# Kernel tuning notes

Hardware: AMD Instinct MI355X
Metric: run time of the kernel (lower is better)

## Reference

```python
import jax, jax.numpy as jnp
import numpy as np

B, N, L, C, H = 8, 300, 4096, 256, 8
DH = C // H  # 32; doubled to 64 after concat with pos/sine embeddings


def _linear_params(key, fan_in, fan_out):
    kw, kb = jax.random.split(key)
    bound = 1.0 / np.sqrt(fan_in)
    W = jax.random.uniform(kw, (fan_out, fan_in), jnp.float32, -bound, bound)
    b = jax.random.uniform(kb, (fan_out,), jnp.float32, -bound, bound)
    return W, b


def setup_inputs() -> dict:
    key = jax.random.key(0)
    ks = jax.random.split(key, 13)
    inp = {
        "query": jax.random.normal(ks[0], (B, N, C), jnp.float32),
        "key": jax.random.normal(ks[1], (B, L, C), jnp.float32),
        "value": jax.random.normal(ks[2], (B, L, C), jnp.float32),
        "query_pos": jax.random.normal(ks[3], (B, N, C), jnp.float32),
        "key_pos": jax.random.normal(ks[4], (B, L, C), jnp.float32),
        "query_sine_embed": jax.random.normal(ks[5], (B, N, C), jnp.float32),
    }
    names = ["qc", "qp", "qs", "kc", "kp", "v", "o"]
    for i, nm in enumerate(names):
        W, b = _linear_params(ks[6 + i], C, C)
        inp[f"W{nm}"] = W
        inp[f"b{nm}"] = b
    return inp


def reference(query, key, value, query_pos, key_pos, query_sine_embed,
              Wqc, bqc, Wqp, bqp, Wqs, bqs, Wkc, bkc, Wkp, bkp, Wv, bv, Wo, bo):
    lin = lambda x, W, b: jnp.einsum("bnc,dc->bnd", x, W) + b
    qc = lin(query, Wqc, bqc)                  # (B, N, C)
    kc = lin(key, Wkc, bkc)                    # (B, L, C)
    v = lin(value, Wv, bv)                     # (B, L, C)
    kp = lin(key_pos, Wkp, bkp)                # (B, L, C)
    qp = lin(query_pos, Wqp, bqp)              # is_first=True branch
    q = qc + qp
    k = kc + kp
    qs = lin(query_sine_embed, Wqs, bqs)
    # split heads and concat content with positional/sine embedding -> head dim 2*DH
    q = jnp.concatenate([q.reshape(B, N, H, DH), qs.reshape(B, N, H, DH)], axis=3)   # (B,N,H,2DH)
    k = jnp.concatenate([k.reshape(B, L, H, DH), kp.reshape(B, L, H, DH)], axis=3)   # (B,L,H,2DH)
    vh = v.reshape(B, L, H, DH)
    scale = (2 * DH) ** -0.5
    attn = jnp.einsum("bnhd,blhd->bhnl", q * scale, k)      # (B,H,N,L)
    attn = jax.nn.softmax(attn, axis=-1)
    out = jnp.einsum("bhnl,blhd->bnhd", attn, vh).reshape(B, N, C)
    out = jnp.einsum("bnc,dc->bnd", out, Wo) + bo
    return query + out  # identity = query
```

## Files before the change

### kernel.cpp

```cpp
#include <hip/hip_runtime.h>
#include <hip/hip_bf16.h>

using bf8_t = __attribute__((ext_vector_type(8))) short;
using bf4_t = __attribute__((ext_vector_type(4))) short;
using u16x4 = __attribute__((ext_vector_type(4))) unsigned short;
using f32x4 = __attribute__((ext_vector_type(4))) float;

constexpr int B_   = 8;
constexpr int N_   = 300;
constexpr int L_   = 4096;
constexpr int C_   = 256;
constexpr int H_   = 8;
constexpr int NPAD = 320;
constexpr int QT_  = 5;
constexpr int SPL_ = 4;
constexpr int TPS_ = 16;
constexpr float SCALE = 0.18033688011112042f;

__device__ __forceinline__ unsigned short f2b(float f) {
  unsigned u = __float_as_uint(f);
  u += 0x7FFFu + ((u >> 16) & 1u);
  return (unsigned short)(u >> 16);
}

__device__ __forceinline__ void stage_cvt16(unsigned short* dst, const float* src) {
#pragma unroll
  for (int half = 0; half < 2; ++half) {
    f32x4 x0 = *(const f32x4*)(src + half * 8);
    f32x4 x1 = *(const f32x4*)(src + half * 8 + 4);
    bf8_t v;
#pragma unroll
    for (int j = 0; j < 4; ++j) { v[j] = (short)f2b(x0[j]); v[4 + j] = (short)f2b(x1[j]); }
    *(bf8_t*)(dst + half * 8) = v;
  }
}

__device__ __forceinline__ void gload_lds16(const void* g, void* l) {
  __builtin_amdgcn_global_load_lds(
      (const __attribute__((address_space(1))) unsigned int*)g,
      (__attribute__((address_space(3))) unsigned int*)l, 16, 0, 0);
}

__device__ __forceinline__ unsigned cvt_pk_bf16(float lo, float hi) {
  unsigned r;
  asm("v_cvt_pk_bf16_f32 %0, %1, %2" : "=v"(r) : "v"(lo), "v"(hi));
  return r;
}

__global__ __launch_bounds__(256) void wcvt_k(
    const float* __restrict__ W0, const float* __restrict__ W1, const float* __restrict__ W2,
    const float* __restrict__ W3, const float* __restrict__ W4, const float* __restrict__ W5,
    unsigned short* __restrict__ Wsw)
{
  const float* W[6] = {W0, W1, W2, W3, W4, W5};
  const int kt = blockIdx.x, i = blockIdx.y;
  const int d = threadIdx.x;
  const float* src = W[i] + (size_t)d * C_ + kt * 64;
  unsigned short* dst = Wsw + ((size_t)(i * 4 + kt) * 256 + d) * 64;
#pragma unroll
  for (int g = 0; g < 8; ++g) {
    f32x4 a = *(const f32x4*)(src + g * 8);
    f32x4 b = *(const f32x4*)(src + g * 8 + 4);
    bf8_t v;
#pragma unroll
    for (int j = 0; j < 4; ++j) { v[j] = (short)f2b(a[j]); v[4 + j] = (short)f2b(b[j]); }
    *(bf8_t*)(dst + (g ^ (d & 7)) * 8) = v;
  }
}

__global__ __launch_bounds__(256, 2) void kvproj_k(
    const float* __restrict__ xp, const float* __restrict__ xk, const float* __restrict__ xv,
    const unsigned short* __restrict__ Wsw,
    const float* __restrict__ bkp, const float* __restrict__ bkc, const float* __restrict__ bv,
    unsigned short* __restrict__ Kc, unsigned short* __restrict__ Kp, unsigned short* __restrict__ Vt)
{
  __shared__ __align__(16) unsigned short Al[2][64 * 64];
  __shared__ __align__(16) unsigned short Bl[2][256 * 64];
  const int tid = threadIdx.x, lane = tid & 63, wv = tid >> 6;
  const int fr = lane & 15, fg = lane >> 4;
  const int row0 = blockIdx.x * 64;
  const int b = row0 >> 12, ll0 = row0 & (L_ - 1);
  const float* Ax[3] = {xp, xk, xv};

  const int sr = tid >> 2, sc = (tid & 3) * 16;
  const int ag = sc >> 3;

  f32x4 acc[16];

  auto stageB = [&](int step, int buf) {
    const char* bsrc = (const char*)Wsw + (size_t)step * 32768;
    char* bdst = (char*)&Bl[buf][0];
#pragma unroll
    for (int c = 0; c < 8; ++c) {
      const int off = c * 4096 + wv * 1024 + lane * 16;
      gload_lds16(bsrc + off, bdst + off);
    }
  };
  auto stageA_load = [&](int step, f32x4* ar) {
    const int i = step >> 2, kt = step & 3;
    const float* src = Ax[i] + ((size_t)(row0 + sr)) * C_ + kt * 64 + sc;
#pragma unroll
    for (int j = 0; j < 4; ++j) ar[j] = *(const f32x4*)(src + j * 4);
  };
  auto stageA_write = [&](int buf, const f32x4* ar) {
    unsigned short* base = &Al[buf][sr * 64];
    bf8_t v0, v1;
#pragma unroll
    for (int j = 0; j < 4; ++j) {
      v0[j] = (short)f2b(ar[0][j]); v0[4 + j] = (short)f2b(ar[1][j]);
      v1[j] = (short)f2b(ar[2][j]); v1[4 + j] = (short)f2b(ar[3][j]);
    }
    *(bf8_t*)(base + ((ag ^ (sr & 7)) * 8))       = v0;
    *(bf8_t*)(base + (((ag | 1) ^ (sr & 7)) * 8)) = v1;
  };

  {
    f32x4 a0[4];
    stageA_load(0, a0);
    stageB(0, 0);
    stageA_write(0, a0);
  }
  __syncthreads();

  int cur = 0;
  const int xrow = wv * 16 + fr;
  const int l_out = ll0 + wv * 16 + fr;
  for (int step = 0; step < 12; ++step) {
    const int i = step >> 2, kt = step & 3;
    if (kt == 0 && i != 1) {
#pragma unroll
      for (int nt = 0; nt < 16; ++nt) acc[nt] = (f32x4){0.f, 0.f, 0.f, 0.f};
    }
    const int nxt = cur ^ 1;
    f32x4 arn[4];
    if (step < 11) {
      stageA_load(step + 1, arn);
      stageB(step + 1, nxt);
    }
    const unsigned short* Ab = &Al[cur][0];
    const unsigned short* Bb = &Bl[cur][0];
#pragma unroll
    for (int kh = 0; kh < 2; ++kh) {
      const int gx = (4 * kh + fg) ^ (fr & 7);
      bf8_t xf = *(const bf8_t*)(Ab + xrow * 64 + gx * 8);
#pragma unroll
      for (int nt = 0; nt < 16; ++nt) {
        bf8_t wf = *(const bf8_t*)(Bb + (nt * 16 + fr) * 64 + gx * 8);
        acc[nt] = __builtin_amdgcn_mfma_f32_16x16x32_bf16(wf, xf, acc[nt], 0, 0, 0);
      }
    }
    if (kt == 3) {
      if (i < 2) {
        unsigned short* outp = (i == 0) ? Kp : Kc;
#pragma unroll
        for (int nt = 0; nt < 16; ++nt) {
          const int d0 = nt * 16 + fg * 4;
          f32x4 bb = *(const f32x4*)(bkp + d0);
          if (i == 1) bb += *(const f32x4*)(bkc + d0);
          u16x4 v;
#pragma unroll
          for (int r = 0; r < 4; ++r) v[r] = f2b(acc[nt][r] + bb[r]);
          *(u16x4*)(outp + ((size_t)(b * H_ + (d0 >> 5)) * L_ + l_out) * 32 + (d0 & 31)) = v;
        }
      } else {
        __syncthreads();
        unsigned short* T = (unsigned short*)&Bl[0][0];
#pragma unroll
        for (int nt = 0; nt < 16; ++nt) {
          const int d0 = nt * 16 + fg * 4;
          f32x4 bb = *(const f32x4*)(bv + d0);
#pragma unroll
          for (int r = 0; r < 4; ++r)
            T[(d0 + r) * 68 + wv * 16 + fr] = f2b(acc[nt][r] + bb[r]);
        }
        __syncthreads();
        const int d = tid, h2 = d >> 5, dh2 = d & 31;
        unsigned short* dst = Vt + ((size_t)(b * H_ + h2) * 32 + dh2) * L_ + ll0;
#pragma unroll
        for (int j = 0; j < 16; ++j)
          *(u16x4*)(dst + j * 4) = *(const u16x4*)(T + d * 68 + j * 4);
      }
    }
    if (step < 11) stageA_write(nxt, arn);
    __syncthreads();
    cur = nxt;
  }
}

__global__ __launch_bounds__(256, 2) void qproj_k(
    const float* __restrict__ xp, const float* __restrict__ xq, const float* __restrict__ xs,
    const unsigned short* __restrict__ Wsw,
    const float* __restrict__ bqp, const float* __restrict__ bqc, const float* __restrict__ bqs,
    unsigned short* __restrict__ Qcat)
{
  __shared__ __align__(16) unsigned short Al[2][64 * 64];
  __shared__ __align__(16) unsigned short Bl[2][256 * 64];
  const int tid = threadIdx.x, lane = tid & 63, wv = tid >> 6;
  const int fr = lane & 15, fg = lane >> 4;
  const int b = blockIdx.x / 5, n0 = (blockIdx.x % 5) * 64;
  const float* Ax[3] = {xp, xq, xs};

  const int sr = tid >> 2, sc = (tid & 3) * 16;
  const int ag = sc >> 3;
  const bool arow_ok = (n0 + sr) < N_;

  f32x4 acc[16];

  auto stageB = [&](int step, int buf) {
    const char* bsrc = (const char*)Wsw + (size_t)(12 + step) * 32768;
    char* bdst = (char*)&Bl[buf][0];
#pragma unroll
    for (int c = 0; c < 8; ++c) {
      const int off = c * 4096 + wv * 1024 + lane * 16;
      gload_lds16(bsrc + off, bdst + off);
    }
  };
  auto stageA_load = [&](int step, f32x4* ar) {
    const int i = step >> 2, kt = step & 3;
    if (arow_ok) {
      const float* src = Ax[i] + ((size_t)b * N_ + n0 + sr) * C_ + kt * 64 + sc;
#pragma unroll
      for (int j = 0; j < 4; ++j) ar[j] = *(const f32x4*)(src + j * 4);
    } else {
#pragma unroll
      for (int j = 0; j < 4; ++j) ar[j] = (f32x4){0.f, 0.f, 0.f, 0.f};
    }
  };
  auto stageA_write = [&](int buf, const f32x4* ar) {
    unsigned short* base = &Al[buf][sr * 64];
    bf8_t v0, v1;
#pragma unroll
    for (int j = 0; j < 4; ++j) {
      v0[j] = (short)f2b(ar[0][j]); v0[4 + j] = (short)f2b(ar[1][j]);
      v1[j] = (short)f2b(ar[2][j]); v1[4 + j] = (short)f2b(ar[3][j]);
    }
    *(bf8_t*)(base + ((ag ^ (sr & 7)) * 8))       = v0;
    *(bf8_t*)(base + (((ag | 1) ^ (sr & 7)) * 8)) = v1;
  };

  {
    f32x4 a0[4];
    stageA_load(0, a0);
    stageB(0, 0);
    stageA_write(0, a0);
  }
  __syncthreads();

  int cur = 0;
  const int xrow = wv * 16 + fr;
  const int n_out = n0 + wv * 16 + fr;
  const bool ok = n_out < N_;
  for (int step = 0; step < 12; ++step) {
    if (step == 0 || step == 8) {
#pragma unroll
      for (int nt = 0; nt < 16; ++nt) acc[nt] = (f32x4){0.f, 0.f, 0.f, 0.f};
    }
    const int nxt = cur ^ 1;
    f32x4 arn[4];
    if (step < 11) {
      stageA_load(step + 1, arn);
      stageB(step + 1, nxt);
    }
    const unsigned short* Ab = &Al[cur][0];
    const unsigned short* Bb = &Bl[cur][0];
#pragma unroll
    for (int kh = 0; kh < 2; ++kh) {
      const int gx = (4 * kh + fg) ^ (fr & 7);
      bf8_t xf = *(const bf8_t*)(Ab + xrow * 64 + gx * 8);
#pragma unroll
      for (int nt = 0; nt < 16; ++nt) {
        bf8_t wf = *(const bf8_t*)(Bb + (nt * 16 + fr) * 64 + gx * 8);
        acc[nt] = __builtin_amdgcn_mfma_f32_16x16x32_bf16(wf, xf, acc[nt], 0, 0, 0);
      }
    }
    if (step == 7 || step == 11) {
      const int off = (step == 7) ? 0 : 32;
#pragma unroll
      for (int nt = 0; nt < 16; ++nt) {
        const int d0 = nt * 16 + fg * 4;
        f32x4 bb;
        if (step == 7) bb = *(const f32x4*)(bqp + d0) + *(const f32x4*)(bqc + d0);
        else           bb = *(const f32x4*)(bqs + d0);
        u16x4 v;
#pragma unroll
        for (int r = 0; r < 4; ++r) v[r] = ok ? f2b((acc[nt][r] + bb[r]) * SCALE) : (unsigned short)0;
        *(u16x4*)(Qcat + ((size_t)(b * H_ + (d0 >> 5)) * NPAD + n_out) * 64 + off + (d0 & 31)) = v;
      }
    }
    if (step < 11) stageA_write(nxt, arn);
    __syncthreads();
    cur = nxt;
  }
}

__global__ __launch_bounds__(256, 5) void attn_k(
    const unsigned short* __restrict__ Qcat, const unsigned short* __restrict__ Kc,
    const unsigned short* __restrict__ Kp, const unsigned short* __restrict__ Vt,
    float* __restrict__ PO, float* __restrict__ PM, float* __restrict__ PLs)
{
  __shared__ __align__(16) unsigned short Kcl[2][64 * 32];
  __shared__ __align__(16) unsigned short Kpl[2][64 * 32];
  __shared__ __align__(16) unsigned short Vp[2][32][72];
  const int x = blockIdx.x;
  const int qt = x >> 8;
  const int rem = x & 255;
  const int s = rem & (SPL_ - 1);
  const int h = (rem >> 2) & (H_ - 1);
  const int b = rem >> 5;
  const int n0 = qt * 64;
  const int tid = threadIdx.x, lane = tid & 63, wv = tid >> 6;
  const int fr = lane & 15, fg = lane >> 4;

  const unsigned short* Qb = Qcat + ((size_t)b * H_ + h) * NPAD * 64;
  bf8_t qf[2];
  {
    const int qrow = n0 + wv * 16 + fr;
    qf[0] = *(const bf8_t*)&Qb[(size_t)qrow * 64 + 8 * fg];
    qf[1] = *(const bf8_t*)&Qb[(size_t)qrow * 64 + 32 + 8 * fg];
  }
  float m_r = -1e30f, l_r = 0.f;
  f32x4 o[2] = {};

  const unsigned short* KcB = Kc + ((size_t)b * H_ + h) * L_ * 32;
  const unsigned short* KpB = Kp + ((size_t)b * H_ + h) * L_ * 32;
  const unsigned short* VB  = Vt + ((size_t)b * H_ + h) * 32 * (size_t)L_;

  const int koff = tid * 16;
  const int vd = tid >> 3, vc = (tid & 7) * 8;

  auto stageK = [&](int t, int buf) {
    gload_lds16((const char*)KcB + (size_t)t * 4096 + koff, (char*)&Kcl[buf][0] + koff);
    gload_lds16((const char*)KpB + (size_t)t * 4096 + koff, (char*)&Kpl[buf][0] + koff);
  };

  const int t0 = s * TPS_, t1 = t0 + TPS_;

  stageK(t0, 0);
  bf8_t vreg = *(const bf8_t*)(VB + (size_t)vd * L_ + t0 * 64 + vc);

  int cur = 0;
  for (int t = t0; t < t1; ++t) {
    *(bf8_t*)&Vp[cur][vd][vc] = vreg;
    __syncthreads();
    if (t + 1 < t1) {
      stageK(t + 1, cur ^ 1);
      vreg = *(const bf8_t*)(VB + (size_t)vd * L_ + (t + 1) * 64 + vc);
    }
    f32x4 sc[4] = {};
#pragma unroll
    for (int nf = 0; nf < 4; ++nf) {
      const int kro = (nf * 16 + fr) * 32 + 8 * fg;
      bf8_t kf0 = *(const bf8_t*)&Kcl[cur][kro];
      bf8_t kf1 = *(const bf8_t*)&Kpl[cur][kro];
      sc[nf] = __builtin_amdgcn_mfma_f32_16x16x32_bf16(kf0, qf[0], sc[nf], 0, 0, 0);
      sc[nf] = __builtin_amdgcn_mfma_f32_16x16x32_bf16(kf1, qf[1], sc[nf], 0, 0, 0);
    }
    float mx = fmaxf(fmaxf(sc[0][0], sc[0][1]), fmaxf(sc[0][2], sc[0][3]));
#pragma unroll
    for (int nf = 1; nf < 4; ++nf)
      mx = fmaxf(mx, fmaxf(fmaxf(sc[nf][0], sc[nf][1]), fmaxf(sc[nf][2], sc[nf][3])));
    mx = fmaxf(mx, __shfl_xor(mx, 16));
    mx = fmaxf(mx, __shfl_xor(mx, 32));
    const float mnew = fmaxf(m_r, mx);
    const float corr = exp2f(m_r - mnew);
    float ps = 0.f;
#pragma unroll
    for (int nf = 0; nf < 4; ++nf)
#pragma unroll
      for (int r = 0; r < 4; ++r) {
        const float p = exp2f(sc[nf][r] - mnew);
        sc[nf][r] = p;
        ps += p;
      }
    ps += __shfl_xor(ps, 16);
    ps += __shfl_xor(ps, 32);
    l_r = l_r * corr + ps;
    m_r = mnew;
#pragma unroll
    for (int r = 0; r < 4; ++r) { o[0][r] *= corr; o[1][r] *= corr; }
    unsigned pw[8];
#pragma unroll
    for (int nf = 0; nf < 4; ++nf) {
      pw[2 * nf]     = cvt_pk_bf16(sc[nf][0], sc[nf][1]);
      pw[2 * nf + 1] = cvt_pk_bf16(sc[nf][2], sc[nf][3]);
    }
#pragma unroll
    for (int kh = 0; kh < 2; ++kh) {
      union { unsigned u[4]; bf8_t v; } pu;
      pu.u[0] = pw[4 * kh];     pu.u[1] = pw[4 * kh + 1];
      pu.u[2] = pw[4 * kh + 2]; pu.u[3] = pw[4 * kh + 3];
      const bf8_t pf = pu.v;
#pragma unroll
      for (int df = 0; df < 2; ++df) {
        const unsigned short* vrow = &Vp[cur][df * 16 + fr][0];
        bf4_t va = *(const bf4_t*)(vrow + kh * 32 + fg * 4);
        bf4_t vb = *(const bf4_t*)(vrow + kh * 32 + 16 + fg * 4);
        bf8_t vf;
#pragma unroll
        for (int j = 0; j < 4; ++j) { vf[j] = va[j]; vf[4 + j] = vb[j]; }
        o[df] = __builtin_amdgcn_mfma_f32_16x16x32_bf16(vf, pf, o[df], 0, 0, 0);
      }
    }
    cur ^= 1;
  }
  const int rec = (((b * H_) + h) * QT_ + qt) * SPL_ + s;
  const int q = wv * 16 + fr;
  if (fg == 0) {
    PM [rec * 64 + q] = m_r;
    PLs[rec * 64 + q] = l_r;
  }
#pragma unroll
  for (int df = 0; df < 2; ++df)
    *(f32x4*)(PO + ((size_t)rec * 64 + q) * 32 + df * 16 + fg * 4) = o[df];
}

__global__ __launch_bounds__(256) void combine_k(
    const float* __restrict__ PO, const float* __restrict__ PM, const float* __restrict__ PLs,
    unsigned short* __restrict__ aout)
{
  const int qt = blockIdx.x, h = blockIdx.y, b = blockIdx.z;
  const int tid = threadIdx.x;
  const int row = tid >> 2, dh0 = (tid & 3) * 8;
  const int rec0 = (((b * H_) + h) * QT_ + qt) * SPL_;
  float m[SPL_], w[SPL_];
  float M = -1e30f;
#pragma unroll
  for (int s = 0; s < SPL_; ++s) { m[s] = PM[(rec0 + s) * 64 + row]; M = fmaxf(M, m[s]); }
  float denom = 0.f;
#pragma unroll
  for (int s = 0; s < SPL_; ++s) {
    w[s] = exp2f(m[s] - M);
    denom += w[s] * PLs[(rec0 + s) * 64 + row];
  }
  float num[8] = {};
#pragma unroll
  for (int s = 0; s < SPL_; ++s) {
    const float* po = PO + ((size_t)(rec0 + s) * 64 + row) * 32 + dh0;
    f32x4 a = *(const f32x4*)po;
    f32x4 c = *(const f32x4*)(po + 4);
#pragma unroll
    for (int j = 0; j < 4; ++j) { num[j] += w[s] * a[j]; num[4 + j] += w[s] * c[j]; }
  }
  const int n = qt * 64 + row;
  if (n < N_) {
    const float inv = 1.f / denom;
    bf8_t v;
#pragma unroll
    for (int j = 0; j < 8; ++j) v[j] = (short)f2b(num[j] * inv);
    *(bf8_t*)(aout + ((size_t)b * NPAD + n) * C_ + h * 32 + dh0) = v;
  }
}

__global__ __launch_bounds__(256) void oproj_k(
    const unsigned short* __restrict__ aout, const float* __restrict__ Wo,
    const float* __restrict__ bo, const float* __restrict__ query,
    float* __restrict__ out)
{
  __shared__ __align__(16) unsigned short Al[64][72];
  __shared__ __align__(16) unsigned short Bl[64][72];
  const int b = blockIdx.z, n0 = blockIdx.y * 64, d0 = blockIdx.x * 64;
  const int tid = threadIdx.x, lane = tid & 63, wv = tid >> 6;
  const int wm = wv >> 1, wn = wv & 1;
  const int sr = tid >> 2, sc = (tid & 3) * 16;
  const int fr = lane & 15, fg = lane >> 4;
  f32x4 acc[2][2] = {};

  for (int kt = 0; kt < 4; ++kt) {
    const int k0 = kt * 64;
    {
      const unsigned short* src = aout + ((size_t)b * NPAD + n0 + sr) * C_ + k0 + sc;
      *(bf8_t*)&Al[sr][sc]     = *(const bf8_t*)src;
      *(bf8_t*)&Al[sr][sc + 8] = *(const bf8_t*)(src + 8);
    }
    stage_cvt16(&Bl[sr][sc], Wo + (size_t)(d0 + sr) * C_ + k0 + sc);
    __syncthreads();
#pragma unroll
    for (int kh = 0; kh < 2; ++kh) {
      const int ko = kh * 32 + 8 * fg;
      bf8_t af[2], bq[2];
#pragma unroll
      for (int m = 0; m < 2; ++m) {
        af[m] = *(const bf8_t*)&Al[wm * 32 + m * 16 + fr][ko];
        bq[m] = *(const bf8_t*)&Bl[wn * 32 + m * 16 + fr][ko];
      }
#pragma unroll
      for (int m = 0; m < 2; ++m)
#pragma unroll
        for (int n = 0; n < 2; ++n)
          acc[m][n] = __builtin_amdgcn_mfma_f32_16x16x32_bf16(af[m], bq[n], acc[m][n], 0, 0, 0);
    }
    __syncthreads();
  }
#pragma unroll
  for (int m = 0; m < 2; ++m)
#pragma unroll
    for (int nn = 0; nn < 2; ++nn) {
      const int d = d0 + wn * 32 + nn * 16 + fr;
      const float bb = bo[d];
#pragma unroll
      for (int r = 0; r < 4; ++r) {
        const int n = n0 + wm * 32 + m * 16 + fg * 4 + r;
        if (n < N_) {
          const size_t gi = ((size_t)b * N_ + n) * C_ + d;
          out[gi] = acc[m][nn][r] + bb + query[gi];
        }
      }
    }
}

extern "C" void kernel_launch(void* const* d_in, const int* in_sizes, int n_in,
                              void* d_out, int out_size, void* d_ws, size_t ws_size,
                              hipStream_t stream)
{
  const float* query = (const float*)d_in[0];
  const float* key   = (const float*)d_in[1];
  const float* value = (const float*)d_in[2];
  const float* qpos  = (const float*)d_in[3];
  const float* kpos  = (const float*)d_in[4];
  const float* qsine = (const float*)d_in[5];
  const float* Wqc = (const float*)d_in[6];  const float* bqc = (const float*)d_in[7];
  const float* Wqp = (const float*)d_in[8];  const float* bqp = (const float*)d_in[9];
  const float* Wqs = (const float*)d_in[10]; const float* bqs = (const float*)d_in[11];
  const float* Wkc = (const float*)d_in[12]; const float* bkc = (const float*)d_in[13];
  const float* Wkp = (const float*)d_in[14]; const float* bkp = (const float*)d_in[15];
  const float* Wv  = (const float*)d_in[16]; const float* bv  = (const float*)d_in[17];
  const float* Wo  = (const float*)d_in[18]; const float* bo  = (const float*)d_in[19];

  const size_t qcat_b = (size_t)B_ * H_ * NPAD * 64 * 2;
  const size_t kc_b   = (size_t)B_ * H_ * L_ * 32 * 2;
  const size_t kp_b   = kc_b;
  const size_t vt_b   = kc_b;
  const size_t aout_b = (size_t)B_ * NPAD * C_ * 2;
  const size_t nrec   = (size_t)B_ * H_ * QT_ * SPL_;
  const size_t po_b   = nrec * 64 * 32 * 4;
  const size_t pm_b   = nrec * 64 * 4;
  const size_t pl_b   = nrec * 64 * 4;
  const size_t wsw_b  = (size_t)24 * 256 * 64 * 2;
  if (ws_size < qcat_b + kc_b + kp_b + vt_b + aout_b + po_b + pm_b + pl_b + wsw_b) return;
  char* ws = (char*)d_ws;
  unsigned short* Qcat = (unsigned short*)(ws);
  unsigned short* Kc   = (unsigned short*)(ws + qcat_b);
  unsigned short* Kp   = (unsigned short*)(ws + qcat_b + kc_b);
  unsigned short* Vt   = (unsigned short*)(ws + qcat_b + kc_b + kp_b);
  unsigned short* aout = (unsigned short*)(ws + qcat_b + kc_b + kp_b + vt_b);
  float* PO  = (float*)(ws + qcat_b + kc_b + kp_b + vt_b + aout_b);
  float* PM  = (float*)(ws + qcat_b + kc_b + kp_b + vt_b + aout_b + po_b);
  float* PLs = (float*)(ws + qcat_b + kc_b + kp_b + vt_b + aout_b + po_b + pm_b);
  unsigned short* Wsw = (unsigned short*)(ws + qcat_b + kc_b + kp_b + vt_b + aout_b + po_b + pm_b + pl_b);
  float* out = (float*)d_out;

  wcvt_k   <<<dim3(4, 6),                256, 0, stream>>>(Wkp, Wkc, Wv, Wqp, Wqc, Wqs, Wsw);
  qproj_k  <<<dim3(B_ * QT_),            256, 0, stream>>>(qpos, query, qsine, Wsw, bqp, bqc, bqs, Qcat);
  kvproj_k <<<dim3(512),                 256, 0, stream>>>(kpos, key, value, Wsw, bkp, bkc, bv, Kc, Kp, Vt);
  attn_k   <<<dim3(QT_ * SPL_ * B_ * H_), 256, 0, stream>>>(Qcat, Kc, Kp, Vt, PO, PM, PLs);
  combine_k<<<dim3(QT_, 8, 8),           256, 0, stream>>>(PO, PM, PLs, aout);
  oproj_k  <<<dim3(4, QT_, 8),           256, 0, stream>>>(aout, Wo, bo, query, out);
}
```

Measured before the change: 138.7 us.

## Split K/V projections across grid via score algebra and retile kvproj

The kernel uses the identity q·(kc+kp) + qs·kp = q·kc + (q+qs)·kp. Kc now stores only the kc projection, and the second half of Qcat carries q+qs instead of qs alone. This removes the accumulation dependency between the kp and kc projections, so kvproj_k launches a 512x3 grid with one projection per block. Each block uses 32-wide K steps, 4x4 MFMA tiles per wave, a smaller shared buffer and higher occupancy. The trade-off is more blocks that each re-stage the activation tile, plus a second weight-conversion kernel with a new 32-column swizzled layout.

```diff
diff --git a/kernel.cpp b/kernel.cpp
--- a/kernel.cpp
+++ b/kernel.cpp
@@ -49,14 +49,13 @@
 
 __global__ __launch_bounds__(256) void wcvt_k(
     const float* __restrict__ W0, const float* __restrict__ W1, const float* __restrict__ W2,
-    const float* __restrict__ W3, const float* __restrict__ W4, const float* __restrict__ W5,
-    unsigned short* __restrict__ Wsw)
-{
-  const float* W[6] = {W0, W1, W2, W3, W4, W5};
+    unsigned short* __restrict__ Wq)
+{
+  const float* W[3] = {W0, W1, W2};
   const int kt = blockIdx.x, i = blockIdx.y;
   const int d = threadIdx.x;
   const float* src = W[i] + (size_t)d * C_ + kt * 64;
-  unsigned short* dst = Wsw + ((size_t)(i * 4 + kt) * 256 + d) * 64;
+  unsigned short* dst = Wq + ((size_t)(i * 4 + kt) * 256 + d) * 64;
 #pragma unroll
   for (int g = 0; g < 8; ++g) {
     f32x4 a = *(const f32x4*)(src + g * 8);
@@ -68,54 +67,71 @@
   }
 }
 
-__global__ __launch_bounds__(256, 2) void kvproj_k(
+__global__ __launch_bounds__(256) void wcvt2_k(
+    const float* __restrict__ W0, const float* __restrict__ W1, const float* __restrict__ W2,
+    unsigned short* __restrict__ Wk)
+{
+  const float* W[3] = {W0, W1, W2};
+  const int kt = blockIdx.x, i = blockIdx.y;
+  const int d = threadIdx.x;
+  const float* src = W[i] + (size_t)d * C_ + kt * 32;
+  unsigned short* dst = Wk + ((size_t)(i * 8 + kt) * 256 + d) * 32;
+#pragma unroll
+  for (int g = 0; g < 4; ++g) {
+    f32x4 a = *(const f32x4*)(src + g * 8);
+    f32x4 b = *(const f32x4*)(src + g * 8 + 4);
+    bf8_t v;
+#pragma unroll
+    for (int j = 0; j < 4; ++j) { v[j] = (short)f2b(a[j]); v[4 + j] = (short)f2b(b[j]); }
+    *(bf8_t*)(dst + (g ^ (d & 3)) * 8) = v;
+  }
+}
+
+__global__ __launch_bounds__(256, 4) void kvproj_k(
     const float* __restrict__ xp, const float* __restrict__ xk, const float* __restrict__ xv,
-    const unsigned short* __restrict__ Wsw,
+    const unsigned short* __restrict__ Wk,
     const float* __restrict__ bkp, const float* __restrict__ bkc, const float* __restrict__ bv,
     unsigned short* __restrict__ Kc, unsigned short* __restrict__ Kp, unsigned short* __restrict__ Vt)
 {
-  __shared__ __align__(16) unsigned short Al[2][64 * 64];
-  __shared__ __align__(16) unsigned short Bl[2][256 * 64];
+  __shared__ __align__(16) unsigned short LB[20480];
   const int tid = threadIdx.x, lane = tid & 63, wv = tid >> 6;
   const int fr = lane & 15, fg = lane >> 4;
+  const int i = blockIdx.y;
   const int row0 = blockIdx.x * 64;
   const int b = row0 >> 12, ll0 = row0 & (L_ - 1);
-  const float* Ax[3] = {xp, xk, xv};
-
-  const int sr = tid >> 2, sc = (tid & 3) * 16;
-  const int ag = sc >> 3;
-
-  f32x4 acc[16];
+  const float* X    = (i == 0) ? xp  : (i == 1) ? xk  : xv;
+  const float* bias = (i == 0) ? bkp : (i == 1) ? bkc : bv;
+
+  const int ar = tid >> 2, ac = tid & 3;
+  const int agx = (ac ^ (ar & 3)) * 8;
+
+  f32x4 acc[4][4] = {};
+
+  const unsigned short* Wi = Wk + (size_t)i * 8 * 8192;
 
   auto stageB = [&](int step, int buf) {
-    const char* bsrc = (const char*)Wsw + (size_t)step * 32768;
-    char* bdst = (char*)&Bl[buf][0];
-#pragma unroll
-    for (int c = 0; c < 8; ++c) {
-      const int off = c * 4096 + wv * 1024 + lane * 16;
-      gload_lds16(bsrc + off, bdst + off);
-    }
-  };
-  auto stageA_load = [&](int step, f32x4* ar) {
-    const int i = step >> 2, kt = step & 3;
-    const float* src = Ax[i] + ((size_t)(row0 + sr)) * C_ + kt * 64 + sc;
-#pragma unroll
-    for (int j = 0; j < 4; ++j) ar[j] = *(const f32x4*)(src + j * 4);
-  };
-  auto stageA_write = [&](int buf, const f32x4* ar) {
-    unsigned short* base = &Al[buf][sr * 64];
-    bf8_t v0, v1;
-#pragma unroll
-    for (int j = 0; j < 4; ++j) {
-      v0[j] = (short)f2b(ar[0][j]); v0[4 + j] = (short)f2b(ar[1][j]);
-      v1[j] = (short)f2b(ar[2][j]); v1[4 + j] = (short)f2b(ar[3][j]);
-    }
-    *(bf8_t*)(base + ((ag ^ (sr & 7)) * 8))       = v0;
-    *(bf8_t*)(base + (((ag | 1) ^ (sr & 7)) * 8)) = v1;
+    const char* src = (const char*)(Wi + step * 8192);
+    char* dst = (char*)(LB + 4096 + buf * 8192);
+#pragma unroll
+    for (int c = 0; c < 4; ++c) {
+      const int off = c * 4096 + tid * 16;
+      gload_lds16(src + off, dst + off);
+    }
+  };
+  auto stageA_load = [&](int step, f32x4* arg) {
+    const float* s = X + (size_t)(row0 + ar) * C_ + step * 32 + ac * 8;
+    arg[0] = *(const f32x4*)s;
+    arg[1] = *(const f32x4*)(s + 4);
+  };
+  auto stageA_write = [&](int buf, const f32x4* arg) {
+    bf8_t v;
+#pragma unroll
+    for (int j = 0; j < 4; ++j) { v[j] = (short)f2b(arg[0][j]); v[4 + j] = (short)f2b(arg[1][j]); }
+    *(bf8_t*)(LB + buf * 2048 + ar * 32 + agx) = v;
   };
 
   {
-    f32x4 a0[4];
+    f32x4 a0[2];
     stageA_load(0, a0);
     stageB(0, 0);
     stageA_write(0, a0);
@@ -123,73 +139,72 @@
   __syncthreads();
 
   int cur = 0;
-  const int xrow = wv * 16 + fr;
-  const int l_out = ll0 + wv * 16 + fr;
-  for (int step = 0; step < 12; ++step) {
-    const int i = step >> 2, kt = step & 3;
-    if (kt == 0 && i != 1) {
-#pragma unroll
-      for (int nt = 0; nt < 16; ++nt) acc[nt] = (f32x4){0.f, 0.f, 0.f, 0.f};
-    }
+  const int gx = (fg ^ (fr & 3)) * 8;
+  for (int step = 0; step < 8; ++step) {
     const int nxt = cur ^ 1;
-    f32x4 arn[4];
-    if (step < 11) {
+    f32x4 arn[2];
+    if (step < 7) {
       stageA_load(step + 1, arn);
       stageB(step + 1, nxt);
     }
-    const unsigned short* Ab = &Al[cur][0];
-    const unsigned short* Bb = &Bl[cur][0];
-#pragma unroll
-    for (int kh = 0; kh < 2; ++kh) {
-      const int gx = (4 * kh + fg) ^ (fr & 7);
-      bf8_t xf = *(const bf8_t*)(Ab + xrow * 64 + gx * 8);
-#pragma unroll
-      for (int nt = 0; nt < 16; ++nt) {
-        bf8_t wf = *(const bf8_t*)(Bb + (nt * 16 + fr) * 64 + gx * 8);
-        acc[nt] = __builtin_amdgcn_mfma_f32_16x16x32_bf16(wf, xf, acc[nt], 0, 0, 0);
-      }
-    }
-    if (kt == 3) {
-      if (i < 2) {
-        unsigned short* outp = (i == 0) ? Kp : Kc;
-#pragma unroll
-        for (int nt = 0; nt < 16; ++nt) {
-          const int d0 = nt * 16 + fg * 4;
-          f32x4 bb = *(const f32x4*)(bkp + d0);
-          if (i == 1) bb += *(const f32x4*)(bkc + d0);
-          u16x4 v;
-#pragma unroll
-          for (int r = 0; r < 4; ++r) v[r] = f2b(acc[nt][r] + bb[r]);
-          *(u16x4*)(outp + ((size_t)(b * H_ + (d0 >> 5)) * L_ + l_out) * 32 + (d0 & 31)) = v;
-        }
-      } else {
-        __syncthreads();
-        unsigned short* T = (unsigned short*)&Bl[0][0];
-#pragma unroll
-        for (int nt = 0; nt < 16; ++nt) {
-          const int d0 = nt * 16 + fg * 4;
-          f32x4 bb = *(const f32x4*)(bv + d0);
-#pragma unroll
-          for (int r = 0; r < 4; ++r)
-            T[(d0 + r) * 68 + wv * 16 + fr] = f2b(acc[nt][r] + bb[r]);
-        }
-        __syncthreads();
-        const int d = tid, h2 = d >> 5, dh2 = d & 31;
-        unsigned short* dst = Vt + ((size_t)(b * H_ + h2) * 32 + dh2) * L_ + ll0;
-#pragma unroll
-        for (int j = 0; j < 16; ++j)
-          *(u16x4*)(dst + j * 4) = *(const u16x4*)(T + d * 68 + j * 4);
-      }
-    }
-    if (step < 11) stageA_write(nxt, arn);
+    const unsigned short* Ab = LB + cur * 2048;
+    const unsigned short* Bb = LB + 4096 + cur * 8192;
+    bf8_t xf[4];
+#pragma unroll
+    for (int mt = 0; mt < 4; ++mt)
+      xf[mt] = *(const bf8_t*)(Ab + (mt * 16 + fr) * 32 + gx);
+#pragma unroll
+    for (int nt = 0; nt < 4; ++nt) {
+      bf8_t wf = *(const bf8_t*)(Bb + (wv * 64 + nt * 16 + fr) * 32 + gx);
+#pragma unroll
+      for (int mt = 0; mt < 4; ++mt)
+        acc[nt][mt] = __builtin_amdgcn_mfma_f32_16x16x32_bf16(wf, xf[mt], acc[nt][mt], 0, 0, 0);
+    }
+    if (step < 7) stageA_write(nxt, arn);
     __syncthreads();
     cur = nxt;
   }
+
+  if (i < 2) {
+    unsigned short* outp = (i == 0) ? Kp : Kc;
+#pragma unroll
+    for (int nt = 0; nt < 4; ++nt) {
+      const int d0 = wv * 64 + nt * 16 + fg * 4;
+      const f32x4 bb = *(const f32x4*)(bias + d0);
+      const int h = d0 >> 5, dh = d0 & 31;
+#pragma unroll
+      for (int mt = 0; mt < 4; ++mt) {
+        const int l = ll0 + mt * 16 + fr;
+        u16x4 v;
+#pragma unroll
+        for (int r = 0; r < 4; ++r) v[r] = f2b(acc[nt][mt][r] + bb[r]);
+        *(u16x4*)(outp + ((size_t)(b * H_ + h) * L_ + l) * 32 + dh) = v;
+      }
+    }
+  } else {
+    unsigned short* T = LB;
+#pragma unroll
+    for (int nt = 0; nt < 4; ++nt) {
+      const int d0 = wv * 64 + nt * 16 + fg * 4;
+      const f32x4 bb = *(const f32x4*)(bias + d0);
+#pragma unroll
+      for (int mt = 0; mt < 4; ++mt)
+#pragma unroll
+        for (int r = 0; r < 4; ++r)
+          T[(d0 + r) * 68 + mt * 16 + fr] = f2b(acc[nt][mt][r] + bb[r]);
+    }
+    __syncthreads();
+    const int d = tid;
+    unsigned short* dst = Vt + ((size_t)(b * H_ + (d >> 5)) * 32 + (d & 31)) * L_ + ll0;
+#pragma unroll
+    for (int j = 0; j < 16; ++j)
+      *(u16x4*)(dst + j * 4) = *(const u16x4*)(T + d * 68 + j * 4);
+  }
 }
 
 __global__ __launch_bounds__(256, 2) void qproj_k(
     const float* __restrict__ xp, const float* __restrict__ xq, const float* __restrict__ xs,
-    const unsigned short* __restrict__ Wsw,
+    const unsigned short* __restrict__ Wq,
     const float* __restrict__ bqp, const float* __restrict__ bqc, const float* __restrict__ bqs,
     unsigned short* __restrict__ Qcat)
 {
@@ -204,10 +219,10 @@
   const int ag = sc >> 3;
   const bool arow_ok = (n0 + sr) < N_;
 
-  f32x4 acc[16];
+  f32x4 acc[16] = {};
 
   auto stageB = [&](int step, int buf) {
-    const char* bsrc = (const char*)Wsw + (size_t)(12 + step) * 32768;
+    const char* bsrc = (const char*)Wq + (size_t)step * 32768;
     char* bdst = (char*)&Bl[buf][0];
 #pragma unroll
     for (int c = 0; c < 8; ++c) {
@@ -251,10 +266,6 @@
   const int n_out = n0 + wv * 16 + fr;
   const bool ok = n_out < N_;
   for (int step = 0; step < 12; ++step) {
-    if (step == 0 || step == 8) {
-#pragma unroll
-      for (int nt = 0; nt < 16; ++nt) acc[nt] = (f32x4){0.f, 0.f, 0.f, 0.f};
-    }
     const int nxt = cur ^ 1;
     f32x4 arn[4];
     if (step < 11) {
@@ -265,11 +276,11 @@
     const unsigned short* Bb = &Bl[cur][0];
 #pragma unroll
     for (int kh = 0; kh < 2; ++kh) {
-      const int gx = (4 * kh + fg) ^ (fr & 7);
-      bf8_t xf = *(const bf8_t*)(Ab + xrow * 64 + gx * 8);
+      const int gxx = (4 * kh + fg) ^ (fr & 7);
+      bf8_t xf = *(const bf8_t*)(Ab + xrow * 64 + gxx * 8);
 #pragma unroll
       for (int nt = 0; nt < 16; ++nt) {
-        bf8_t wf = *(const bf8_t*)(Bb + (nt * 16 + fr) * 64 + gx * 8);
+        bf8_t wf = *(const bf8_t*)(Bb + (nt * 16 + fr) * 64 + gxx * 8);
         acc[nt] = __builtin_amdgcn_mfma_f32_16x16x32_bf16(wf, xf, acc[nt], 0, 0, 0);
       }
     }
@@ -278,9 +289,8 @@
 #pragma unroll
       for (int nt = 0; nt < 16; ++nt) {
         const int d0 = nt * 16 + fg * 4;
-        f32x4 bb;
-        if (step == 7) bb = *(const f32x4*)(bqp + d0) + *(const f32x4*)(bqc + d0);
-        else           bb = *(const f32x4*)(bqs + d0);
+        f32x4 bb = *(const f32x4*)(bqp + d0) + *(const f32x4*)(bqc + d0);
+        if (step == 11) bb += *(const f32x4*)(bqs + d0);
         u16x4 v;
 #pragma unroll
         for (int r = 0; r < 4; ++r) v[r] = ok ? f2b((acc[nt][r] + bb[r]) * SCALE) : (unsigned short)0;
@@ -546,13 +556,15 @@
   float* PO  = (float*)(ws + qcat_b + kc_b + kp_b + vt_b + aout_b);
   float* PM  = (float*)(ws + qcat_b + kc_b + kp_b + vt_b + aout_b + po_b);
   float* PLs = (float*)(ws + qcat_b + kc_b + kp_b + vt_b + aout_b + po_b + pm_b);
-  unsigned short* Wsw = (unsigned short*)(ws + qcat_b + kc_b + kp_b + vt_b + aout_b + po_b + pm_b + pl_b);
+  unsigned short* Wq = (unsigned short*)(ws + qcat_b + kc_b + kp_b + vt_b + aout_b + po_b + pm_b + pl_b);
+  unsigned short* Wk = Wq + (size_t)12 * 16384;
   float* out = (float*)d_out;
 
-  wcvt_k   <<<dim3(4, 6),                256, 0, stream>>>(Wkp, Wkc, Wv, Wqp, Wqc, Wqs, Wsw);
-  qproj_k  <<<dim3(B_ * QT_),            256, 0, stream>>>(qpos, query, qsine, Wsw, bqp, bqc, bqs, Qcat);
-  kvproj_k <<<dim3(512),                 256, 0, stream>>>(kpos, key, value, Wsw, bkp, bkc, bv, Kc, Kp, Vt);
+  wcvt_k   <<<dim3(4, 3),                 256, 0, stream>>>(Wqp, Wqc, Wqs, Wq);
+  wcvt2_k  <<<dim3(8, 3),                 256, 0, stream>>>(Wkp, Wkc, Wv, Wk);
+  qproj_k  <<<dim3(B_ * QT_),             256, 0, stream>>>(qpos, query, qsine, Wq, bqp, bqc, bqs, Qcat);
+  kvproj_k <<<dim3(512, 3),               256, 0, stream>>>(kpos, key, value, Wk, bkp, bkc, bv, Kc, Kp, Vt);
   attn_k   <<<dim3(QT_ * SPL_ * B_ * H_), 256, 0, stream>>>(Qcat, Kc, Kp, Vt, PO, PM, PLs);
-  combine_k<<<dim3(QT_, 8, 8),           256, 0, stream>>>(PO, PM, PLs, aout);
-  oproj_k  <<<dim3(4, QT_, 8),           256, 0, stream>>>(aout, Wo, bo, query, out);
-}
+  combine_k<<<dim3(QT_, 8, 8),            256, 0, stream>>>(PO, PM, PLs, aout);
+  oproj_k  <<<dim3(4, QT_, 8),            256, 0, stream>>>(aout, Wo, bo, query, out);
+}
```

New measurement: 131.4 us. 5.3% less time.
